# Kernel tuning notes

Measured on AMD Instinct MI355X. Metric: run time of the kernel, lower is better.

## Reference

```python
import jax, jax.numpy as jnp
import numpy as np

N = 8192
D_IN = 256
D_HID = 256
D_OUT = 256


def setup_inputs() -> dict:
    key = jax.random.key(0)
    k_x, k_a, k_q, k_k, k_v = jax.random.split(key, 5)
    X = jax.random.normal(k_x, (N, D_IN), dtype=jnp.float32)
    # binary adjacency, zero diagonal (module adds self-loops via +eye)
    A = jax.random.randint(k_a, (N, N), 0, 2, dtype=jnp.int32)
    A = A * (1 - jnp.eye(N, dtype=jnp.int32))
    # parameters: randn / 10, as in the torch __init__
    Wq = jax.random.normal(k_q, (D_IN, D_HID), dtype=jnp.float32) / 10.0
    Wk = jax.random.normal(k_k, (D_IN, D_HID), dtype=jnp.float32) / 10.0
    Wv = jax.random.normal(k_v, (D_IN, D_OUT), dtype=jnp.float32) / 10.0
    return {"X": X, "A": A, "Wq": Wq, "Wk": Wk, "Wv": Wv}


def reference(X, A, Wq, Wk, Wv):
    n = A.shape[0]
    Af = A.astype(X.dtype) + jnp.eye(n, dtype=X.dtype)  # add self-loops
    Q = X @ Wq  # [N, H]
    K = X @ Wk  # [N, H]
    V = X @ Wv  # [N, O]
    S = Q @ K.T  # [N, N]
    # torch: nan_to_num(-inf*(1-A), nan=0) -> 0 where A==1, finite-min where A==0
    mask = jnp.nan_to_num(-jnp.inf * (1.0 - Af), nan=0.0)
    P = jax.nn.softmax(S + mask, axis=1)
    return P @ V  # [N, O]
```

## Files before the change

### kernel.cpp

```cpp
#include <hip/hip_runtime.h>
#include <stdint.h>


typedef _Float16 f16;
typedef unsigned short u16;
typedef __attribute__((ext_vector_type(8))) _Float16 f16x8;
typedef __attribute__((ext_vector_type(4))) _Float16 f16x4;
typedef __attribute__((ext_vector_type(4))) float f32x4;

#define NN 8192
#define DD 256
#define BR 64
#define BC 64
#define CCH 4
#define COLS (NN / CCH)
#define NIT (COLS / BC)

#define MFMA(a, b, c) __builtin_amdgcn_mfma_f32_16x16x32_f16((a), (b), (c), 0, 0, 0)

__device__ __forceinline__ void gl2lds16(const void* g, void* l) {
    __builtin_amdgcn_global_load_lds(
        (const __attribute__((address_space(1))) unsigned int*)g,
        (__attribute__((address_space(3))) unsigned int*)l, 16, 0, 0);
}

__device__ __forceinline__ u16 f16bits(f16 h) {
    union { f16 h; u16 u; } c;
    c.h = h;
    return c.u;
}

__global__ void splitX_kernel(const float4* __restrict__ X, f16x4* __restrict__ Xh,
                              f16x4* __restrict__ Xl) {
    const int i = blockIdx.x * blockDim.x + threadIdx.x;
    const float4 v = X[i];
    const f16 h0 = (f16)v.x, h1 = (f16)v.y, h2 = (f16)v.z, h3 = (f16)v.w;
    f16x4 H = {h0, h1, h2, h3};
    f16x4 L = {(f16)(v.x - (float)h0), (f16)(v.y - (float)h1), (f16)(v.z - (float)h2),
               (f16)(v.w - (float)h3)};
    Xh[i] = H;
    Xl[i] = L;
}

__global__ void splitW_kernel(const float* __restrict__ Wq, const float* __restrict__ Wk,
                              const float* __restrict__ Wv, f16* __restrict__ WtH,
                              f16* __restrict__ WtL) {
    const int i = blockIdx.x * blockDim.x + threadIdx.x;
    const int mat = i >> 16;
    const int k = (i >> 8) & 255;
    const int n = i & 255;
    const float* W = (mat == 0) ? Wq : ((mat == 1) ? Wk : Wv);
    const float v = W[k * 256 + n];
    const f16 h = (f16)v;
    const size_t o = (size_t)(mat * 256 + n) * 256 + k;
    WtH[o] = h;
    WtL[o] = (f16)(v - (float)h);
}

__global__ __launch_bounds__(256, 2) void qkv_kernel(
    const f16* __restrict__ Xh, const f16* __restrict__ Xl,
    const f16* __restrict__ WtH, const f16* __restrict__ WtL,
    f16* __restrict__ Qh, f16* __restrict__ Ql,
    f16* __restrict__ Kh, f16* __restrict__ Vt) {
    __shared__ f16 Wh[64 * 256];
    __shared__ f16 Wl[64 * 256];
    const int lane = threadIdx.x & 63;
    const int w = threadIdx.x >> 6;
    const int l15 = lane & 15;
    const int quad = lane >> 4;
    const int r0 = blockIdx.x * 64;
    const int mat = blockIdx.y;

    f16x8 xh[8], xl[8];
    const size_t xb = (size_t)(r0 + w * 16 + l15) * DD + quad * 8;
#pragma unroll
    for (int kc = 0; kc < 8; ++kc) {
        xh[kc] = *(const f16x8*)(Xh + xb + kc * 32);
        xl[kc] = *(const f16x8*)(Xl + xb + kc * 32);
    }
    const int orow = r0 + w * 16 + quad * 4;

#pragma unroll 1
    for (int c = 0; c < 4; ++c) {
        const int nb = mat * 256 + c * 64;
#pragma unroll
        for (int i = 0; i < 8; ++i) {
            const int r = w * 16 + i * 2 + (lane >> 5);
            gl2lds16(WtH + (size_t)(nb + r) * DD + (((lane & 31) ^ (r & 7)) * 8),
                     &Wh[(w * 16 + i * 2) * 256]);
        }
#pragma unroll
        for (int i = 0; i < 8; ++i) {
            const int r = w * 16 + i * 2 + (lane >> 5);
            gl2lds16(WtL + (size_t)(nb + r) * DD + (((lane & 31) ^ (r & 7)) * 8),
                     &Wl[(w * 16 + i * 2) * 256]);
        }
        __syncthreads();

        const f32x4 fzero = {0.f, 0.f, 0.f, 0.f};
        f32x4 acc[4];
#pragma unroll
        for (int nt = 0; nt < 4; ++nt) acc[nt] = fzero;
#pragma unroll
        for (int kc = 0; kc < 8; ++kc)
#pragma unroll
            for (int nt = 0; nt < 4; ++nt) {
                const int r = nt * 16 + l15;
                const int blk = (((kc * 4 + quad) ^ (r & 7)) * 8);
                const f16x8 wh = *(const f16x8*)&Wh[r * 256 + blk];
                const f16x8 wl = *(const f16x8*)&Wl[r * 256 + blk];
                acc[nt] = MFMA(xh[kc], wh, acc[nt]);
                acc[nt] = MFMA(xh[kc], wl, acc[nt]);
                acc[nt] = MFMA(xl[kc], wh, acc[nt]);
            }

        if (mat == 0) {
#pragma unroll
            for (int nt = 0; nt < 4; ++nt)
#pragma unroll
                for (int rg = 0; rg < 4; ++rg) {
                    const int col = c * 64 + nt * 16 + l15;
                    const float v = acc[nt][rg];
                    const f16 h = (f16)v;
                    Qh[(size_t)(orow + rg) * DD + col] = h;
                    Ql[(size_t)(orow + rg) * DD + col] = (f16)(v - (float)h);
                }
        } else if (mat == 1) {
#pragma unroll
            for (int nt = 0; nt < 4; ++nt)
#pragma unroll
                for (int rg = 0; rg < 4; ++rg) {
                    const int col = c * 64 + nt * 16 + l15;
                    Kh[(size_t)(orow + rg) * DD + col] = (f16)acc[nt][rg];
                }
        } else {
#pragma unroll
            for (int nt = 0; nt < 4; ++nt) {
                const int n = c * 64 + nt * 16 + l15;
                ushort4 pk;
                pk.x = f16bits((f16)acc[nt][0]);
                pk.y = f16bits((f16)acc[nt][1]);
                pk.z = f16bits((f16)acc[nt][2]);
                pk.w = f16bits((f16)acc[nt][3]);
                *(ushort4*)(Vt + (size_t)n * NN + orow) = pk;
            }
        }
        __syncthreads();
    }
}

__global__ __launch_bounds__(256, 2) void flash_kernel(
    const f16* __restrict__ Qh, const f16* __restrict__ Ql,
    const f16* __restrict__ Kh, const f16* __restrict__ Vt,
    const int* __restrict__ A,
    float* __restrict__ pO, float* __restrict__ pM, float* __restrict__ pL) {
    __shared__ f16 Klds[64 * 256];
    __shared__ f16 Vlds[256 * 64];
    __shared__ f16 Plds[4][16 * 88];

    const int lane = threadIdx.x & 63;
    const int w = threadIdx.x >> 6;
    const int l15 = lane & 15;
    const int quad = lane >> 4;
    const int bid = blockIdx.x;
    const int cch = bid & 3;
    const int r0 = (bid >> 2) * BR;
    const int col0 = cch * COLS;

    f16x8 qh[8], ql[8];
    {
        const size_t qb = (size_t)(r0 + w * 16 + l15) * DD + quad * 8;
#pragma unroll
        for (int kc = 0; kc < 8; ++kc) {
            qh[kc] = *(const f16x8*)(Qh + qb + kc * 32);
            ql[kc] = *(const f16x8*)(Ql + qb + kc * 32);
        }
    }

    const f32x4 fzero = {0.f, 0.f, 0.f, 0.f};
    f32x4 accO[16];
#pragma unroll
    for (int i = 0; i < 16; ++i) accO[i] = fzero;
    float mrow[4], lrow[4];
#pragma unroll
    for (int r = 0; r < 4; ++r) {
        mrow[r] = -1e30f;
        lrow[r] = 0.f;
    }
    const int growb = r0 + w * 16 + quad * 4;
    f16* Pw = &Plds[w][0];

#pragma unroll 1
    for (int it = 0; it < NIT; ++it) {
        const int j0 = col0 + it * BC;

#pragma unroll
        for (int i = 0; i < 8; ++i) {
            const int r = w * 16 + i * 2 + (lane >> 5);
            gl2lds16(Kh + (size_t)(j0 + r) * DD + (((lane & 31) ^ (r & 7)) * 8),
                     &Klds[(w * 16 + i * 2) * 256]);
        }
#pragma unroll
        for (int i = 0; i < 8; ++i) {
            const int n = w * 64 + i * 8 + (lane >> 3);
            gl2lds16(Vt + (size_t)n * NN + j0 + (((lane & 7) ^ ((lane >> 3) & 7)) * 8),
                     &Vlds[(w * 64 + i * 8) * 64]);
        }
        __syncthreads();

        int av[4][4];
#pragma unroll
        for (int rgi = 0; rgi < 4; ++rgi)
#pragma unroll
            for (int jt = 0; jt < 4; ++jt)
                av[rgi][jt] = A[(size_t)(growb + rgi) * NN + j0 + jt * 16 + l15];

        f32x4 accS[4];
#pragma unroll
        for (int jt = 0; jt < 4; ++jt) accS[jt] = fzero;
#pragma unroll
        for (int kc = 0; kc < 8; ++kc)
#pragma unroll
            for (int jt = 0; jt < 4; ++jt) {
                const int r = jt * 16 + l15;
                const f16x8 kf =
                    *(const f16x8*)&Klds[r * 256 + (((kc * 4 + quad) ^ (r & 7)) * 8)];
                accS[jt] = MFMA(qh[kc], kf, accS[jt]);
                accS[jt] = MFMA(ql[kc], kf, accS[jt]);
            }

        float alpha[4];
#pragma unroll
        for (int rgi = 0; rgi < 4; ++rgi) {
            const int gr = growb + rgi;
            float mx = -3.0e38f;
#pragma unroll
            for (int jt = 0; jt < 4; ++jt) {
                const int gc = j0 + jt * 16 + l15;
                float s = (av[rgi][jt] != 0 || gr == gc) ? accS[jt][rgi] : -3.0e38f;
                accS[jt][rgi] = s;
                mx = fmaxf(mx, s);
            }
#pragma unroll
            for (int off = 1; off < 16; off <<= 1) mx = fmaxf(mx, __shfl_xor(mx, off, 64));
            const float mnew = fmaxf(mrow[rgi], mx);
            alpha[rgi] = __expf(mrow[rgi] - mnew);
            mrow[rgi] = mnew;
            float rs = 0.f;
#pragma unroll
            for (int jt = 0; jt < 4; ++jt) {
                const float s = accS[jt][rgi];
                const float e = (s > -1.0e37f) ? __expf(s - mnew) : 0.f;
                rs += e;
                Pw[(quad * 4 + rgi) * 88 + jt * 16 + l15] = (f16)e;
            }
#pragma unroll
            for (int off = 1; off < 16; off <<= 1) rs += __shfl_xor(rs, off, 64);
            lrow[rgi] = lrow[rgi] * alpha[rgi] + rs;
        }
#pragma unroll
        for (int nt = 0; nt < 16; ++nt)
#pragma unroll
            for (int rgi = 0; rgi < 4; ++rgi) accO[nt][rgi] *= alpha[rgi];

        f16x8 pf[2];
        pf[0] = *(const f16x8*)&Pw[l15 * 88 + quad * 8];
        pf[1] = *(const f16x8*)&Pw[l15 * 88 + 32 + quad * 8];

#pragma unroll
        for (int nt = 0; nt < 16; ++nt)
#pragma unroll
            for (int kc2 = 0; kc2 < 2; ++kc2) {
                const int n = nt * 16 + l15;
                const f16x8 vf =
                    *(const f16x8*)&Vlds[n * 64 + (((kc2 * 4 + quad) ^ (n & 7)) * 8)];
                accO[nt] = MFMA(pf[kc2], vf, accO[nt]);
            }
        __syncthreads();
    }

#pragma unroll
    for (int nt = 0; nt < 16; ++nt)
#pragma unroll
        for (int rgi = 0; rgi < 4; ++rgi)
            pO[((size_t)cch * NN + growb + rgi) * DD + nt * 16 + l15] = accO[nt][rgi];
    if (l15 == 0) {
#pragma unroll
        for (int rgi = 0; rgi < 4; ++rgi) {
            pM[(size_t)cch * NN + growb + rgi] = mrow[rgi];
            pL[(size_t)cch * NN + growb + rgi] = lrow[rgi];
        }
    }
}

__global__ __launch_bounds__(256) void merge_kernel(const float* __restrict__ pO,
                                                    const float* __restrict__ pM,
                                                    const float* __restrict__ pL,
                                                    float* __restrict__ out) {
    const int n = threadIdx.x;
#pragma unroll 1
    for (int rr = 0; rr < 8; ++rr) {
        const int row = blockIdx.x * 8 + rr;
        float mc[CCH], lc[CCH];
        float M = -3e38f;
#pragma unroll
        for (int c = 0; c < CCH; ++c) {
            mc[c] = pM[(size_t)c * NN + row];
            lc[c] = pL[(size_t)c * NN + row];
            M = fmaxf(M, mc[c]);
        }
        float L = 0.f, acc = 0.f;
#pragma unroll
        for (int c = 0; c < CCH; ++c) {
            const float wgt = __expf(mc[c] - M);
            L += wgt * lc[c];
            acc += wgt * pO[((size_t)c * NN + row) * DD + n];
        }
        out[(size_t)row * DD + n] = acc / L;
    }
}

extern "C" void kernel_launch(void* const* d_in, const int* in_sizes, int n_in,
                              void* d_out, int out_size, void* d_ws, size_t ws_size,
                              hipStream_t stream) {
    const float* X = (const float*)d_in[0];
    const int* A = (const int*)d_in[1];
    const float* Wq = (const float*)d_in[2];
    const float* Wk = (const float*)d_in[3];
    const float* Wv = (const float*)d_in[4];
    float* out = (float*)d_out;

    char* ws = (char*)d_ws;
    const size_t MB = 1ull << 20;
    f16* Xh = (f16*)(ws + 0 * MB);
    f16* Xl = (f16*)(ws + 4 * MB);
    f16* WtH = (f16*)(ws + 8 * MB);
    f16* WtL = (f16*)(ws + 8 * MB + 512 * 1024);
    f16* Qh = (f16*)(ws + 9 * MB);
    f16* Ql = (f16*)(ws + 13 * MB);
    f16* Kh = (f16*)(ws + 17 * MB);
    f16* Vt = (f16*)(ws + 21 * MB);
    float* pO = (float*)(ws + 25 * MB);
    float* pM = (float*)(ws + 57 * MB);
    float* pL = (float*)(ws + 57 * MB + 256 * 1024);
    (void)ws_size; (void)in_sizes; (void)n_in; (void)out_size;

    splitX_kernel<<<2048, 256, 0, stream>>>((const float4*)X, (f16x4*)Xh, (f16x4*)Xl);
    splitW_kernel<<<768, 256, 0, stream>>>(Wq, Wk, Wv, WtH, WtL);
    qkv_kernel<<<dim3(NN / 64, 3), 256, 0, stream>>>(Xh, Xl, WtH, WtL, Qh, Ql, Kh, Vt);
    flash_kernel<<<(NN / BR) * CCH, 256, 0, stream>>>(Qh, Ql, Kh, Vt, A, pO, pM, pL);
    merge_kernel<<<NN / 8, 256, 0, stream>>>(pO, pM, pL, out);
}
```

Measured before the change: 596.8 us.

## Reuse K LDS for P tile, defer row-sum reduction, pack max shuffles in f16

Drops the separate P buffer and writes the softmax probabilities into the K tile region after the QK^T MFMAs are done, guarded by a new barrier. Moves the adjacency loads before the first barrier as nontemporal loads. Row-sum shuffles leave the per-tile loop and run once at the end. Row-max reductions use packed f16 pairs to halve shuffle count, at the risk of precision loss in the running max. This targets lower LDS footprint, fewer cross-lane shuffles and better latency hiding, but adds an extra barrier per tile.

Measured after the change: 557.3 us. 6.6% less time.

```diff
diff --git a/kernel.cpp b/kernel.cpp
--- a/kernel.cpp
+++ b/kernel.cpp
@@ -18,6 +18,8 @@
 
 #define MFMA(a, b, c) __builtin_amdgcn_mfma_f32_16x16x32_f16((a), (b), (c), 0, 0, 0)
 
+#define LGKM_BARRIER() __asm__ __volatile__("s_waitcnt lgkmcnt(0)\ns_barrier" ::: "memory")
+
 __device__ __forceinline__ void gl2lds16(const void* g, void* l) {
     __builtin_amdgcn_global_load_lds(
         (const __attribute__((address_space(1))) unsigned int*)g,
@@ -29,6 +31,13 @@
     c.h = h;
     return c.u;
 }
+
+union F16x2U {
+    unsigned u;
+    struct { f16 lo, hi; } f;
+};
+
+__device__ __forceinline__ int pswz(int row) { return (row ^ (row >> 2)) & 7; }
 
 __global__ void splitX_kernel(const float4* __restrict__ X, f16x4* __restrict__ Xh,
                               f16x4* __restrict__ Xl) {
@@ -156,7 +165,6 @@
     float* __restrict__ pO, float* __restrict__ pM, float* __restrict__ pL) {
     __shared__ f16 Klds[64 * 256];
     __shared__ f16 Vlds[256 * 64];
-    __shared__ f16 Plds[4][16 * 88];
 
     const int lane = threadIdx.x & 63;
     const int w = threadIdx.x >> 6;
@@ -181,14 +189,13 @@
     f32x4 accO[16];
 #pragma unroll
     for (int i = 0; i < 16; ++i) accO[i] = fzero;
-    float mrow[4], lrow[4];
+    float mrow[4], lpart[4];
 #pragma unroll
     for (int r = 0; r < 4; ++r) {
         mrow[r] = -1e30f;
-        lrow[r] = 0.f;
-    }
-    const int growb = r0 + w * 16 + quad * 4;
-    f16* Pw = &Plds[w][0];
+        lpart[r] = 0.f;
+    }
+    const int srow = r0 + w * 16 + quad * 4;
 
 #pragma unroll 1
     for (int it = 0; it < NIT; ++it) {
@@ -203,17 +210,19 @@
 #pragma unroll
         for (int i = 0; i < 8; ++i) {
             const int n = w * 64 + i * 8 + (lane >> 3);
-            gl2lds16(Vt + (size_t)n * NN + j0 + (((lane & 7) ^ ((lane >> 3) & 7)) * 8),
+            gl2lds16(Vt + (size_t)n * NN + j0 + (((lane & 7) ^ (n & 7)) * 8),
                      &Vlds[(w * 64 + i * 8) * 64]);
         }
+
+        int av[4][4];
+#pragma unroll
+        for (int rgi = 0; rgi < 4; ++rgi)
+#pragma unroll
+            for (int jt = 0; jt < 4; ++jt)
+                av[rgi][jt] = __builtin_nontemporal_load(
+                    A + (size_t)(srow + rgi) * NN + j0 + jt * 16 + l15);
+
         __syncthreads();
-
-        int av[4][4];
-#pragma unroll
-        for (int rgi = 0; rgi < 4; ++rgi)
-#pragma unroll
-            for (int jt = 0; jt < 4; ++jt)
-                av[rgi][jt] = A[(size_t)(growb + rgi) * NN + j0 + jt * 16 + l15];
 
         f32x4 accS[4];
 #pragma unroll
@@ -229,34 +238,61 @@
                 accS[jt] = MFMA(ql[kc], kf, accS[jt]);
             }
 
-        float alpha[4];
+        LGKM_BARRIER();
+
+        float mx[4];
 #pragma unroll
         for (int rgi = 0; rgi < 4; ++rgi) {
-            const int gr = growb + rgi;
-            float mx = -3.0e38f;
+            const int gr = srow + rgi;
+            float m = -3.0e38f;
 #pragma unroll
             for (int jt = 0; jt < 4; ++jt) {
                 const int gc = j0 + jt * 16 + l15;
-                float s = (av[rgi][jt] != 0 || gr == gc) ? accS[jt][rgi] : -3.0e38f;
+                const float s = (av[rgi][jt] != 0 || gr == gc) ? accS[jt][rgi] : -3.0e38f;
                 accS[jt][rgi] = s;
-                mx = fmaxf(mx, s);
-            }
-#pragma unroll
-            for (int off = 1; off < 16; off <<= 1) mx = fmaxf(mx, __shfl_xor(mx, off, 64));
-            const float mnew = fmaxf(mrow[rgi], mx);
+                m = fmaxf(m, s);
+            }
+            mx[rgi] = m;
+        }
+        {
+            F16x2U a, b;
+            a.f.lo = (f16)mx[0];
+            a.f.hi = (f16)mx[1];
+            b.f.lo = (f16)mx[2];
+            b.f.hi = (f16)mx[3];
+#pragma unroll
+            for (int off = 1; off < 16; off <<= 1) {
+                F16x2U as, bs;
+                as.u = __shfl_xor(a.u, off, 64);
+                bs.u = __shfl_xor(b.u, off, 64);
+                a.f.lo = (as.f.lo > a.f.lo) ? as.f.lo : a.f.lo;
+                a.f.hi = (as.f.hi > a.f.hi) ? as.f.hi : a.f.hi;
+                b.f.lo = (bs.f.lo > b.f.lo) ? bs.f.lo : b.f.lo;
+                b.f.hi = (bs.f.hi > b.f.hi) ? bs.f.hi : b.f.hi;
+            }
+            mx[0] = (float)a.f.lo;
+            mx[1] = (float)a.f.hi;
+            mx[2] = (float)b.f.lo;
+            mx[3] = (float)b.f.hi;
+        }
+
+        float alpha[4];
+#pragma unroll
+        for (int rgi = 0; rgi < 4; ++rgi) {
+            const float mnew = fmaxf(mrow[rgi], mx[rgi]);
             alpha[rgi] = __expf(mrow[rgi] - mnew);
             mrow[rgi] = mnew;
             float rs = 0.f;
+            const int lrow = w * 16 + quad * 4 + rgi;
 #pragma unroll
             for (int jt = 0; jt < 4; ++jt) {
                 const float s = accS[jt][rgi];
                 const float e = (s > -1.0e37f) ? __expf(s - mnew) : 0.f;
                 rs += e;
-                Pw[(quad * 4 + rgi) * 88 + jt * 16 + l15] = (f16)e;
-            }
-#pragma unroll
-            for (int off = 1; off < 16; off <<= 1) rs += __shfl_xor(rs, off, 64);
-            lrow[rgi] = lrow[rgi] * alpha[rgi] + rs;
+                const int col = jt * 16 + l15;
+                Klds[lrow * 256 + (((col >> 3) ^ pswz(lrow)) * 8) + (col & 7)] = (f16)e;
+            }
+            lpart[rgi] = lpart[rgi] * alpha[rgi] + rs;
         }
 #pragma unroll
         for (int nt = 0; nt < 16; ++nt)
@@ -264,8 +300,11 @@
             for (int rgi = 0; rgi < 4; ++rgi) accO[nt][rgi] *= alpha[rgi];
 
         f16x8 pf[2];
-        pf[0] = *(const f16x8*)&Pw[l15 * 88 + quad * 8];
-        pf[1] = *(const f16x8*)&Pw[l15 * 88 + 32 + quad * 8];
+        {
+            const int rr = w * 16 + l15;
+            pf[0] = *(const f16x8*)&Klds[rr * 256 + (((0 + quad) ^ pswz(rr)) * 8)];
+            pf[1] = *(const f16x8*)&Klds[rr * 256 + (((4 + quad) ^ pswz(rr)) * 8)];
+        }
 
 #pragma unroll
         for (int nt = 0; nt < 16; ++nt)
@@ -276,19 +315,26 @@
                     *(const f16x8*)&Vlds[n * 64 + (((kc2 * 4 + quad) ^ (n & 7)) * 8)];
                 accO[nt] = MFMA(pf[kc2], vf, accO[nt]);
             }
+
         __syncthreads();
     }
 
 #pragma unroll
+    for (int rgi = 0; rgi < 4; ++rgi)
+#pragma unroll
+        for (int off = 1; off < 16; off <<= 1)
+            lpart[rgi] += __shfl_xor(lpart[rgi], off, 64);
+
+#pragma unroll
     for (int nt = 0; nt < 16; ++nt)
 #pragma unroll
         for (int rgi = 0; rgi < 4; ++rgi)
-            pO[((size_t)cch * NN + growb + rgi) * DD + nt * 16 + l15] = accO[nt][rgi];
+            pO[((size_t)cch * NN + srow + rgi) * DD + nt * 16 + l15] = accO[nt][rgi];
     if (l15 == 0) {
 #pragma unroll
         for (int rgi = 0; rgi < 4; ++rgi) {
-            pM[(size_t)cch * NN + growb + rgi] = mrow[rgi];
-            pL[(size_t)cch * NN + growb + rgi] = lrow[rgi];
+            pM[(size_t)cch * NN + srow + rgi] = mrow[rgi];
+            pL[(size_t)cch * NN + srow + rgi] = lpart[rgi];
         }
     }
 }
```
